# Kernel tuning notes

Hardware: AMD Instinct MI355X
Metric: run time of the kernel (lower is better)

Reference implementation:

```python
import jax, jax.numpy as jnp
import numpy as np

LN_EPS = 1e-5


def _segment_mean(vals, idx, num_segments):
    s = jax.ops.segment_sum(vals, idx, num_segments=num_segments)
    cnt = jax.ops.segment_sum(jnp.ones((vals.shape[0],), vals.dtype), idx, num_segments=num_segments)
    return s / jnp.maximum(cnt, 1.0)[:, None]


def _sage_layer(x, src, dst, W_l, b_l, W_r, gamma, beta):
    # PyG SAGEConv (mean aggr): out = lin_l(mean_{j in N(i)} x_j) + lin_r(x_i)
    N = x.shape[0]
    agg = _segment_mean(x[src], dst, N)                     # [N, in]
    h = agg @ W_l.T + b_l + x @ W_r.T                       # [N, out]
    mu = jnp.mean(h, axis=-1, keepdims=True)
    var = jnp.mean((h - mu) ** 2, axis=-1, keepdims=True)
    h = (h - mu) * jax.lax.rsqrt(var + LN_EPS) * gamma + beta
    return jax.nn.relu(h)                                   # dropout: eval mode (identity)


def setup_inputs() -> dict:
    key = jax.random.key(0)
    ks = jax.random.split(key, 20)
    N, E, IN, H, OUT, G, C = 50000, 600000, 128, 128, 64, 64, 2

    def glorot(k, fo, fi):
        lim = np.sqrt(6.0 / (fo + fi)).astype(np.float32)
        return jax.random.uniform(k, (fo, fi), jnp.float32, -lim, lim)

    inp = {
        'x': jax.random.normal(ks[0], (N, IN), jnp.float32),
        'edge_index': jax.random.randint(ks[1], (2, E), 0, N, jnp.int64),
        'batch': jnp.sort(jax.random.randint(ks[2], (N,), 0, G, jnp.int64)),
    }
    dims = [(IN, H), (H, H), (H, OUT)]
    for i, (fi, fo) in enumerate(dims):
        inp[f'Wl{i}'] = glorot(ks[3 + 4 * i], fo, fi)
        inp[f'bl{i}'] = jnp.zeros((fo,), jnp.float32)
        inp[f'Wr{i}'] = glorot(ks[4 + 4 * i], fo, fi)
        inp[f'g{i}'] = jnp.ones((fo,), jnp.float32)
        inp[f'be{i}'] = jnp.zeros((fo,), jnp.float32)
    inp['cW1'] = glorot(ks[16], H, 2 * OUT)
    inp['cb1'] = jnp.zeros((H,), jnp.float32)
    inp['cW2'] = glorot(ks[17], C, H)
    inp['cb2'] = jnp.zeros((C,), jnp.float32)
    return inp


def reference(x, edge_index, batch,
              Wl0, bl0, Wr0, g0, be0,
              Wl1, bl1, Wr1, g1, be1,
              Wl2, bl2, Wr2, g2, be2,
              cW1, cb1, cW2, cb2):
    src, dst = edge_index[0], edge_index[1]
    h = _sage_layer(x, src, dst, Wl0, bl0, Wr0, g0, be0)
    h = _sage_layer(h, src, dst, Wl1, bl1, Wr1, g1, be1)
    h = _sage_layer(h, src, dst, Wl2, bl2, Wr2, g2, be2)
    G = 64  # number of graphs
    x_mean = _segment_mean(h, batch, G)                     # [G, out]
    x_max = jax.ops.segment_max(h, batch, num_segments=G)   # [G, out]
    z = jnp.concatenate([x_mean, x_max], axis=-1)           # [G, 2*out]
    z = jax.nn.relu(z @ cW1.T + cb1)
    return z @ cW2.T + cb2                                  # [G, num_classes]
```

## Files before the change

### kernel.cpp

```cpp
#include <hip/hip_runtime.h>

typedef unsigned short ushort_t;
typedef short s16x8 __attribute__((ext_vector_type(8)));
typedef float f32x4 __attribute__((ext_vector_type(4)));

#define LN_EPS 1e-5f

__device__ __forceinline__ float b2f(ushort_t u) {
    return __uint_as_float(((unsigned)u) << 16);
}
__device__ __forceinline__ ushort_t f2b(float f) {
    unsigned b = __float_as_uint(f);
    b += 0x7FFFu + ((b >> 16) & 1u);
    return (ushort_t)(b >> 16);
}
__device__ __forceinline__ unsigned f2b2(float lo, float hi) {
    return (unsigned)f2b(lo) | ((unsigned)f2b(hi) << 16);
}
__device__ __forceinline__ float ldf(const void* p, size_t i, int isF) {
    return isF ? ((const float*)p)[i] : b2f(((const ushort_t*)p)[i]);
}

__global__ void GraphSAGE_36026185678961_kernel() {}

__global__ void k_detect_zero(const void* w0, const void* ei, int* __restrict__ flags,
                              int* __restrict__ deg, float* __restrict__ Z, int N) {
    int i = blockIdx.x * blockDim.x + threadIdx.x;
    if (i < N) deg[i] = 0;
    if (i < 64 * 128) Z[i] = 0.f;
    if (blockIdx.x == 0 && threadIdx.x < 64) {
        int t = threadIdx.x;
        const ushort_t* u = (const ushort_t*)w0;
        int pass = 0;
        #pragma unroll
        for (int k = 0; k < 4; ++k) {
            ushort_t v = u[t * 4 + k];
            int ex = (v >> 7) & 0xFF;
            if (ex == 0 || (ex >= 0x60 && ex <= 0x7E)) pass++;
        }
        const unsigned* w = (const unsigned*)ei;
        int nz = (w[2 * t + 1] != 0u) ? 1 : 0;
        #pragma unroll
        for (int off = 32; off; off >>= 1) {
            pass += __shfl_down(pass, off, 64);
            nz += __shfl_down(nz, off, 64);
        }
        if (t == 0) {
            flags[0] = (pass < 205) ? 1 : 0;
            flags[1] = (nz == 0) ? 1 : 0;
        }
    }
}

__global__ void k_xconv(const void* X, const int* __restrict__ flags,
                        ushort_t* __restrict__ XB, int total4) {
    int idx = blockIdx.x * blockDim.x + threadIdx.x;
    if (idx >= total4) return;
    if (flags[0]) {
        float4 v = ((const float4*)X)[idx];
        ushort4 o;
        o.x = f2b(v.x); o.y = f2b(v.y); o.z = f2b(v.z); o.w = f2b(v.w);
        ((ushort4*)XB)[idx] = o;
    } else {
        ((ushort4*)XB)[idx] = ((const ushort4*)X)[idx];
    }
}

__global__ void k_hist(const void* ei, int E, int N, const int* __restrict__ flags,
                       int* __restrict__ deg) {
    int e = blockIdx.x * blockDim.x + threadIdx.x;
    if (e >= E) return;
    int d = flags[1] ? (int)((const long long*)ei)[E + e] : ((const int*)ei)[E + e];
    if ((unsigned)d < (unsigned)N) atomicAdd(&deg[d], 1);
}

__global__ void k_scan1(const int* __restrict__ deg, int N,
                        int* __restrict__ rowptr, int* __restrict__ bsum) {
    __shared__ int wsum[4];
    __shared__ int wpre[4];
    int tid = threadIdx.x;
    int lane = tid & 63;
    int w = tid >> 6;
    int i = blockIdx.x * 256 + tid;
    int v = (i < N) ? deg[i] : 0;
    int x = v;
    #pragma unroll
    for (int off = 1; off < 64; off <<= 1) {
        int t = __shfl_up(x, off, 64);
        if (lane >= off) x += t;
    }
    if (lane == 63) wsum[w] = x;
    __syncthreads();
    if (tid == 0) {
        int a = wsum[0]; wpre[0] = a;
        a += wsum[1]; wpre[1] = a;
        a += wsum[2]; wpre[2] = a;
        a += wsum[3]; wpre[3] = a;
    }
    __syncthreads();
    int woff = (w == 0) ? 0 : wpre[w - 1];
    if (i < N) rowptr[i] = woff + x - v;
    if (tid == 0) bsum[blockIdx.x] = wpre[3];
}

__global__ void k_scan2(const int* __restrict__ bsum, int nb,
                        int* __restrict__ boff, int* __restrict__ rowptrN,
                        const void* batch, int N, int G, const int* __restrict__ flags,
                        int* __restrict__ bounds) {
    __shared__ int wsum[4];
    __shared__ int wpre[4];
    int tid = threadIdx.x;
    int lane = tid & 63;
    int w = tid >> 6;
    int run = 0;
    for (int base = 0; base < nb; base += 256) {
        int i = base + tid;
        int v = (i < nb) ? bsum[i] : 0;
        int x = v;
        #pragma unroll
        for (int off = 1; off < 64; off <<= 1) {
            int t = __shfl_up(x, off, 64);
            if (lane >= off) x += t;
        }
        if (lane == 63) wsum[w] = x;
        __syncthreads();
        if (tid == 0) {
            int a = wsum[0]; wpre[0] = a;
            a += wsum[1]; wpre[1] = a;
            a += wsum[2]; wpre[2] = a;
            a += wsum[3]; wpre[3] = a;
        }
        __syncthreads();
        int woff = (w == 0) ? 0 : wpre[w - 1];
        if (i < nb) boff[i] = run + woff + x - v;
        int tot = wpre[3];
        __syncthreads();
        run += tot;
    }
    if (tid == 0) *rowptrN = run;
    if (tid <= G) {
        int isL = flags[1];
        int lo = 0, hi = N;
        while (lo < hi) {
            int mid = (lo + hi) >> 1;
            int bv = isL ? (int)((const long long*)batch)[mid] : ((const int*)batch)[mid];
            if (bv < tid) lo = mid + 1; else hi = mid;
        }
        bounds[tid] = lo;
    }
}

__global__ void k_scan3(int* __restrict__ rowptr, const int* __restrict__ boff,
                        int* __restrict__ cursor, int N) {
    int i = blockIdx.x * 256 + threadIdx.x;
    if (i < N) {
        int r = rowptr[i] + boff[i >> 8];
        rowptr[i] = r;
        cursor[i] = r;
    }
}

__global__ void k_fill(const void* ei, int E, int N, const int* __restrict__ flags,
                       int* __restrict__ cursor, int* __restrict__ col) {
    int e = blockIdx.x * blockDim.x + threadIdx.x;
    if (e >= E) return;
    int s, d;
    if (flags[1]) {
        const long long* p = (const long long*)ei;
        s = (int)p[e];
        d = (int)p[E + e];
    } else {
        const int* p = (const int*)ei;
        s = p[e];
        d = p[E + e];
    }
    if ((unsigned)d < (unsigned)N) {
        int p = atomicAdd(&cursor[d], 1);
        if ((unsigned)p < (unsigned)E) col[p] = ((unsigned)s < (unsigned)N) ? s : 0;
    }
}

__global__ __launch_bounds__(256) void k_agg(
    const ushort_t* __restrict__ X, const int* __restrict__ rowptr,
    const int* __restrict__ col, ushort_t* __restrict__ AGG, int N) {
    int i = blockIdx.x * 4 + (threadIdx.x >> 6);
    if (i >= N) return;
    int l = threadIdx.x & 63;
    int qn = l >> 4;
    int fo = l & 15;
    const uint4* X8 = (const uint4*)X;
    int s = rowptr[i], e = rowptr[i + 1];
    float al[4] = {0.f, 0.f, 0.f, 0.f};
    float ah[4] = {0.f, 0.f, 0.f, 0.f};
    int p = s + qn;
    for (; p + 4 < e; p += 8) {
        int j0 = col[p], j1 = col[p + 4];
        uint4 u0 = X8[(size_t)j0 * 16 + fo];
        uint4 u1 = X8[(size_t)j1 * 16 + fo];
        unsigned w0[4] = {u0.x, u0.y, u0.z, u0.w};
        unsigned w1[4] = {u1.x, u1.y, u1.z, u1.w};
        #pragma unroll
        for (int k = 0; k < 4; ++k) {
            al[k] += __uint_as_float(w0[k] << 16) + __uint_as_float(w1[k] << 16);
            ah[k] += __uint_as_float(w0[k] & 0xFFFF0000u) + __uint_as_float(w1[k] & 0xFFFF0000u);
        }
    }
    for (; p < e; p += 4) {
        int j = col[p];
        uint4 u = X8[(size_t)j * 16 + fo];
        unsigned w0[4] = {u.x, u.y, u.z, u.w};
        #pragma unroll
        for (int k = 0; k < 4; ++k) {
            al[k] += __uint_as_float(w0[k] << 16);
            ah[k] += __uint_as_float(w0[k] & 0xFFFF0000u);
        }
    }
    #pragma unroll
    for (int k = 0; k < 4; ++k) {
        al[k] += __shfl_xor(al[k], 16, 64);
        al[k] += __shfl_xor(al[k], 32, 64);
        ah[k] += __shfl_xor(ah[k], 16, 64);
        ah[k] += __shfl_xor(ah[k], 32, 64);
    }
    if (qn == 0) {
        int d = e - s;
        float inv = 1.f / (float)(d > 0 ? d : 1);
        uint4 o;
        o.x = f2b2(al[0] * inv, ah[0] * inv);
        o.y = f2b2(al[1] * inv, ah[1] * inv);
        o.z = f2b2(al[2] * inv, ah[2] * inv);
        o.w = f2b2(al[3] * inv, ah[3] * inv);
        ((uint4*)AGG)[(size_t)i * 16 + fo] = o;
    }
}

__global__ void k_wprep(const void* Wl0, const void* Wr0, const void* Wl1, const void* Wr1,
                        const void* Wl2, const void* Wr2, const int* __restrict__ flags,
                        ushort_t* __restrict__ Wb0, ushort_t* __restrict__ Wb1,
                        ushort_t* __restrict__ Wb2) {
    int t = blockIdx.x * blockDim.x + threadIdx.x;
    int isF = flags[0];
    const void* Wl;
    const void* Wr;
    ushort_t* Wb;
    int base;
    if (t < 256 * 128) { Wl = Wl0; Wr = Wr0; Wb = Wb0; base = t; }
    else if (t < 2 * 256 * 128) { Wl = Wl1; Wr = Wr1; Wb = Wb1; base = t - 256 * 128; }
    else if (t < 2 * 256 * 128 + 256 * 64) { Wl = Wl2; Wr = Wr2; Wb = Wb2; base = t - 2 * 256 * 128; }
    else return;
    int f = base >> 8, k = base & 255;
    float v = (k < 128) ? ldf(Wl, f * 128 + k, isF) : ldf(Wr, f * 128 + (k - 128), isF);
    Wb[base] = isF ? f2b(v) : ((const ushort_t*)((k < 128) ? Wl : Wr))[f * 128 + (k & 127)];
}

template <int FO>
__global__ __launch_bounds__(256, 2) void k_gemm_ln(
    const ushort_t* __restrict__ AGG, const ushort_t* __restrict__ X,
    const ushort_t* __restrict__ Wb,
    const void* bl, const void* gam, const void* bet,
    const int* __restrict__ flags,
    ushort_t* __restrict__ H, int M) {
    constexpr int NT = FO / 16;
    constexpr int R = 2;
    int lane = threadIdx.x & 63;
    int wid = threadIdx.x >> 6;
    int wrow0 = (blockIdx.x * 4 + wid) * (R * 16);
    if (wrow0 >= M) return;
    int isF = flags[0];
    int m = lane & 15;
    int q = lane >> 4;

    int arow[R];
    #pragma unroll
    for (int r = 0; r < R; ++r) {
        int ar = wrow0 + r * 16 + m;
        arow[r] = (ar < M) ? ar : (M - 1);
    }

    f32x4 acc[R][NT];
    #pragma unroll
    for (int r = 0; r < R; ++r)
        #pragma unroll
        for (int nt = 0; nt < NT; ++nt) acc[r][nt] = (f32x4){0.f, 0.f, 0.f, 0.f};

    #pragma unroll
    for (int kk = 0; kk < 8; ++kk) {
        const ushort_t* base = (kk < 4) ? AGG : X;
        int ko = (kk & 3) * 32 + q * 8;
        s16x8 a[R];
        #pragma unroll
        for (int r = 0; r < R; ++r)
            a[r] = *(const s16x8*)(base + (size_t)arow[r] * 128 + ko);
        #pragma unroll
        for (int nt = 0; nt < NT; ++nt) {
            s16x8 b = *(const s16x8*)(Wb + (size_t)(nt * 16 + m) * 256 + kk * 32 + q * 8);
            #pragma unroll
            for (int r = 0; r < R; ++r)
                acc[r][nt] = __builtin_amdgcn_mfma_f32_16x16x32_bf16(a[r], b, acc[r][nt], 0, 0, 0);
        }
    }

    #pragma unroll
    for (int r = 0; r < R; ++r) {
        #pragma unroll
        for (int nt = 0; nt < NT; ++nt) {
            float bv = ldf(bl, nt * 16 + m, isF);
            #pragma unroll
            for (int rr = 0; rr < 4; ++rr) acc[r][nt][rr] += bv;
        }
        float mu[4], rs[4];
        #pragma unroll
        for (int rr = 0; rr < 4; ++rr) {
            float s1 = 0.f, s2 = 0.f;
            #pragma unroll
            for (int nt = 0; nt < NT; ++nt) {
                float v = acc[r][nt][rr];
                s1 += v;
                s2 += v * v;
            }
            #pragma unroll
            for (int off = 1; off < 16; off <<= 1) {
                s1 += __shfl_xor(s1, off, 64);
                s2 += __shfl_xor(s2, off, 64);
            }
            float mm = s1 / (float)FO;
            float var = s2 / (float)FO - mm * mm;
            var = var > 0.f ? var : 0.f;
            mu[rr] = mm;
            rs[rr] = rsqrtf(var + LN_EPS);
        }
        #pragma unroll
        for (int nt = 0; nt < NT; ++nt) {
            int n0 = nt * 16 + m;
            float g = ldf(gam, n0, isF);
            float be = ldf(bet, n0, isF);
            #pragma unroll
            for (int rr = 0; rr < 4; ++rr) {
                int row = wrow0 + r * 16 + q * 4 + rr;
                if (row < M) {
                    float y = (acc[r][nt][rr] - mu[rr]) * rs[rr] * g + be;
                    y = y > 0.f ? y : 0.f;
                    H[(size_t)row * FO + n0] = f2b(y);
                }
            }
        }
    }
}

__global__ __launch_bounds__(256) void k_pool(
    const ushort_t* __restrict__ H,
    const int* __restrict__ bounds, float* __restrict__ Z, int N) {
    int g = blockIdx.x >> 4;
    int chunk = blockIdx.x & 15;
    int lane = threadIdx.x & 31;
    int sub = threadIdx.x >> 5;
    int strm = chunk * 8 + sub;
    int s = bounds[g], e = bounds[g + 1];
    s = s < 0 ? 0 : (s > N ? N : s);
    e = e < s ? s : (e > N ? N : e);
    const unsigned* H2 = (const unsigned*)H;
    float sl = 0.f, sh = 0.f, ml = 0.f, mh = 0.f;
    for (int i = s + strm; i < e; i += 128) {
        unsigned u = H2[(size_t)i * 32 + lane];
        float vl = __uint_as_float(u << 16);
        float vh = __uint_as_float(u & 0xFFFF0000u);
        sl += vl; sh += vh;
        ml = ml > vl ? ml : vl;
        mh = mh > vh ? mh : vh;
    }
    int f0 = lane * 2;
    atomicAdd(&Z[g * 128 + f0], sl);
    atomicAdd(&Z[g * 128 + f0 + 1], sh);
    atomicMax((int*)&Z[g * 128 + 64 + f0], __float_as_int(ml));
    atomicMax((int*)&Z[g * 128 + 64 + f0 + 1], __float_as_int(mh));
}

__global__ void k_mlp(const float* __restrict__ Z, const int* __restrict__ bounds,
                      const void* cW1, const void* cb1, const void* cW2, const void* cb2,
                      const int* __restrict__ flags, void* __restrict__ out) {
    int g = blockIdx.x;
    int f = threadIdx.x;
    int isF = flags[0];
    __shared__ float z[128];
    __shared__ float hid[128];
    __shared__ float r0[2], r1[2];
    int cnt = bounds[g + 1] - bounds[g];
    float c = (float)(cnt > 0 ? cnt : 1);
    float zv = Z[g * 128 + f];
    if (f < 64) zv /= c;
    z[f] = zv;
    __syncthreads();
    float acc = ldf(cb1, f, isF);
    #pragma unroll 8
    for (int k = 0; k < 128; ++k) acc += z[k] * ldf(cW1, f * 128 + k, isF);
    acc = acc > 0.f ? acc : 0.f;
    hid[f] = acc;
    __syncthreads();
    float p0 = hid[f] * ldf(cW2, f, isF);
    float p1 = hid[f] * ldf(cW2, 128 + f, isF);
    #pragma unroll
    for (int off = 32; off > 0; off >>= 1) {
        p0 += __shfl_xor(p0, off, 64);
        p1 += __shfl_xor(p1, off, 64);
    }
    int w = f >> 6;
    if ((f & 63) == 0) { r0[w] = p0; r1[w] = p1; }
    __syncthreads();
    if (f == 0) {
        float v0 = r0[0] + r0[1] + ldf(cb2, 0, isF);
        float v1 = r1[0] + r1[1] + ldf(cb2, 1, isF);
        if (isF) {
            ((float*)out)[g * 2 + 0] = v0;
            ((float*)out)[g * 2 + 1] = v1;
        } else {
            ((ushort_t*)out)[g * 2 + 0] = f2b(v0);
            ((ushort_t*)out)[g * 2 + 1] = f2b(v1);
        }
    }
}

extern "C" void kernel_launch(void* const* d_in, const int* in_sizes, int n_in,
                              void* d_out, int out_size, void* d_ws, size_t ws_size,
                              hipStream_t stream) {
    const void* x = d_in[0];
    const void* ei = d_in[1];
    const void* batch = d_in[2];
    const void* Wl0 = d_in[3];
    const void* bl0 = d_in[4];
    const void* Wr0 = d_in[5];
    const void* g0 = d_in[6];
    const void* be0 = d_in[7];
    const void* Wl1 = d_in[8];
    const void* bl1 = d_in[9];
    const void* Wr1 = d_in[10];
    const void* g1 = d_in[11];
    const void* be1 = d_in[12];
    const void* Wl2 = d_in[13];
    const void* bl2 = d_in[14];
    const void* Wr2 = d_in[15];
    const void* g2 = d_in[16];
    const void* be2 = d_in[17];
    const void* cW1 = d_in[18];
    const void* cb1 = d_in[19];
    const void* cW2 = d_in[20];
    const void* cb2 = d_in[21];

    const int N = in_sizes[0] / 128;
    const int E = in_sizes[1] / 2;
    const int G = 64;

    char* w = (char*)d_ws;
    size_t o = 0;
    auto take = [&](size_t bytes) -> void* {
        void* p = w + o;
        o = (o + bytes + 255) & ~(size_t)255;
        return p;
    };
    int nb1 = (N + 255) / 256;
    int* flags  = (int*)take(4 * 4);
    int* rowptr = (int*)take((size_t)(N + 1) * 4);
    int* cursor = (int*)take((size_t)N * 4);
    int* deg    = (int*)take((size_t)N * 4);
    int* bsum   = (int*)take((size_t)nb1 * 4);
    int* boff   = (int*)take((size_t)nb1 * 4);
    int* col    = (int*)take((size_t)E * 4);
    int* bounds = (int*)take((size_t)(G + 1) * 4);
    float* Z    = (float*)take((size_t)G * 128 * 4);
    ushort_t* Wb0 = (ushort_t*)take((size_t)128 * 256 * 2);
    ushort_t* Wb1 = (ushort_t*)take((size_t)128 * 256 * 2);
    ushort_t* Wb2 = (ushort_t*)take((size_t)64 * 256 * 2);
    ushort_t* AGG = (ushort_t*)take((size_t)N * 128 * 2);
    ushort_t* H1  = (ushort_t*)take((size_t)N * 128 * 2);
    ushort_t* H2  = (ushort_t*)take((size_t)N * 128 * 2);
    ushort_t* XB  = H2;
    ushort_t* H3  = H1;
    if (o > ws_size) return;

    int eb = (E + 255) / 256;
    k_detect_zero<<<nb1, 256, 0, stream>>>(Wl0, ei, flags, deg, Z, N);
    k_xconv<<<(N * 128 / 4 + 255) / 256, 256, 0, stream>>>(x, flags, XB, N * 128 / 4);
    k_hist<<<eb, 256, 0, stream>>>(ei, E, N, flags, deg);
    k_scan1<<<nb1, 256, 0, stream>>>(deg, N, rowptr, bsum);
    k_scan2<<<1, 256, 0, stream>>>(bsum, nb1, boff, rowptr + N, batch, N, G, flags, bounds);
    k_scan3<<<nb1, 256, 0, stream>>>(rowptr, boff, cursor, N);
    k_fill<<<eb, 256, 0, stream>>>(ei, E, N, flags, cursor, col);
    k_wprep<<<(2 * 256 * 128 + 256 * 64 + 255) / 256, 256, 0, stream>>>(
        Wl0, Wr0, Wl1, Wr1, Wl2, Wr2, flags, Wb0, Wb1, Wb2);

    int gb = (N + 127) / 128;
    int ab = (N + 3) / 4;

    k_agg<<<ab, 256, 0, stream>>>(XB, rowptr, col, AGG, N);
    k_gemm_ln<128><<<gb, 256, 0, stream>>>(AGG, XB, Wb0, bl0, g0, be0, flags, H1, N);
    k_agg<<<ab, 256, 0, stream>>>(H1, rowptr, col, AGG, N);
    k_gemm_ln<128><<<gb, 256, 0, stream>>>(AGG, H1, Wb1, bl1, g1, be1, flags, H2, N);
    k_agg<<<ab, 256, 0, stream>>>(H2, rowptr, col, AGG, N);
    k_gemm_ln<64><<<gb, 256, 0, stream>>>(AGG, H2, Wb2, bl2, g2, be2, flags, H3, N);

    k_pool<<<G * 16, 256, 0, stream>>>(H3, bounds, Z, N);
    k_mlp<<<G, 128, 0, stream>>>(Z, bounds, cW1, cb1, cW2, cb2, flags, d_out);
}
```

Measured before the change: 376.8 us.

## Transform-then-aggregate in last SAGE layer and merge prep kernels

The last layer now multiplies node features by the stacked [Wl2;Wr2] first, producing a 128-wide T. It then gathers and averages only the 64-wide Wl part over neighbours and fuses bias, self term, LayerNorm and ReLU into the aggregation kernel. This halves the gather width for layer 3 and drops the separate AGG round trip. It also merges the x conversion, degree histogram and weight prep into a single launch. The cost is that neighbour sums are taken over bf16-rounded projected values rather than raw features, which changes rounding slightly.

Result: no change. 377.1 us (+0.1%).

```diff
diff --git a/kernel.cpp b/kernel.cpp
--- a/kernel.cpp
+++ b/kernel.cpp
@@ -52,26 +52,55 @@
     }
 }
 
-__global__ void k_xconv(const void* X, const int* __restrict__ flags,
-                        ushort_t* __restrict__ XB, int total4) {
-    int idx = blockIdx.x * blockDim.x + threadIdx.x;
-    if (idx >= total4) return;
-    if (flags[0]) {
-        float4 v = ((const float4*)X)[idx];
-        ushort4 o;
-        o.x = f2b(v.x); o.y = f2b(v.y); o.z = f2b(v.z); o.w = f2b(v.w);
-        ((ushort4*)XB)[idx] = o;
+__global__ void k_prep(const void* X, ushort_t* __restrict__ XB, int total4, int xb,
+                       const void* ei, int E, int N, int* __restrict__ deg, int eb,
+                       const void* Wl0, const void* Wr0, const void* Wl1, const void* Wr1,
+                       const void* Wl2, const void* Wr2,
+                       ushort_t* __restrict__ Wb0, ushort_t* __restrict__ Wb1,
+                       ushort_t* __restrict__ Wb2,
+                       const int* __restrict__ flags) {
+    int b = blockIdx.x;
+    if (b < xb) {
+        int idx = b * 256 + threadIdx.x;
+        if (idx >= total4) return;
+        if (flags[0]) {
+            float4 v = ((const float4*)X)[idx];
+            ushort4 o;
+            o.x = f2b(v.x); o.y = f2b(v.y); o.z = f2b(v.z); o.w = f2b(v.w);
+            ((ushort4*)XB)[idx] = o;
+        } else {
+            ((ushort4*)XB)[idx] = ((const ushort4*)X)[idx];
+        }
+    } else if (b < xb + eb) {
+        int e = (b - xb) * 256 + threadIdx.x;
+        if (e >= E) return;
+        int d = flags[1] ? (int)((const long long*)ei)[E + e] : ((const int*)ei)[E + e];
+        if ((unsigned)d < (unsigned)N) atomicAdd(&deg[d], 1);
     } else {
-        ((ushort4*)XB)[idx] = ((const ushort4*)X)[idx];
-    }
-}
-
-__global__ void k_hist(const void* ei, int E, int N, const int* __restrict__ flags,
-                       int* __restrict__ deg) {
-    int e = blockIdx.x * blockDim.x + threadIdx.x;
-    if (e >= E) return;
-    int d = flags[1] ? (int)((const long long*)ei)[E + e] : ((const int*)ei)[E + e];
-    if ((unsigned)d < (unsigned)N) atomicAdd(&deg[d], 1);
+        int t = (b - xb - eb) * 256 + threadIdx.x;
+        int isF = flags[0];
+        if (t < 2 * 32768) {
+            const void* Wl = (t < 32768) ? Wl0 : Wl1;
+            const void* Wr = (t < 32768) ? Wr0 : Wr1;
+            ushort_t* Wb = (t < 32768) ? Wb0 : Wb1;
+            int base = t & 32767;
+            int f = base >> 8, k = base & 255;
+            if (isF) {
+                float v = (k < 128) ? ((const float*)Wl)[f * 128 + k]
+                                    : ((const float*)Wr)[f * 128 + (k - 128)];
+                Wb[base] = f2b(v);
+            } else {
+                Wb[base] = ((const ushort_t*)((k < 128) ? Wl : Wr))[f * 128 + (k & 127)];
+            }
+        } else if (t < 2 * 32768 + 16384) {
+            int base = t - 2 * 32768;
+            int f = base >> 7, k = base & 127;
+            const void* W = (f < 64) ? Wl2 : Wr2;
+            int fr = f & 63;
+            Wb2[base] = isF ? f2b(((const float*)W)[fr * 128 + k])
+                            : ((const ushort_t*)W)[fr * 128 + k];
+        }
+    }
 }
 
 __global__ void k_scan1(const int* __restrict__ deg, int N,
@@ -234,25 +263,6 @@
     }
 }
 
-__global__ void k_wprep(const void* Wl0, const void* Wr0, const void* Wl1, const void* Wr1,
-                        const void* Wl2, const void* Wr2, const int* __restrict__ flags,
-                        ushort_t* __restrict__ Wb0, ushort_t* __restrict__ Wb1,
-                        ushort_t* __restrict__ Wb2) {
-    int t = blockIdx.x * blockDim.x + threadIdx.x;
-    int isF = flags[0];
-    const void* Wl;
-    const void* Wr;
-    ushort_t* Wb;
-    int base;
-    if (t < 256 * 128) { Wl = Wl0; Wr = Wr0; Wb = Wb0; base = t; }
-    else if (t < 2 * 256 * 128) { Wl = Wl1; Wr = Wr1; Wb = Wb1; base = t - 256 * 128; }
-    else if (t < 2 * 256 * 128 + 256 * 64) { Wl = Wl2; Wr = Wr2; Wb = Wb2; base = t - 2 * 256 * 128; }
-    else return;
-    int f = base >> 8, k = base & 255;
-    float v = (k < 128) ? ldf(Wl, f * 128 + k, isF) : ldf(Wr, f * 128 + (k - 128), isF);
-    Wb[base] = isF ? f2b(v) : ((const ushort_t*)((k < 128) ? Wl : Wr))[f * 128 + (k & 127)];
-}
-
 template <int FO>
 __global__ __launch_bounds__(256, 2) void k_gemm_ln(
     const ushort_t* __restrict__ AGG, const ushort_t* __restrict__ X,
@@ -344,6 +354,141 @@
                 }
             }
         }
+    }
+}
+
+__global__ __launch_bounds__(256, 2) void k_gemm3(
+    const ushort_t* __restrict__ X,
+    const ushort_t* __restrict__ Wb,
+    ushort_t* __restrict__ T,
+    int M) {
+    constexpr int NT = 8;
+    constexpr int R = 2;
+    int lane = threadIdx.x & 63;
+    int wid = threadIdx.x >> 6;
+    int wrow0 = (blockIdx.x * 4 + wid) * (R * 16);
+    if (wrow0 >= M) return;
+    int m = lane & 15;
+    int q = lane >> 4;
+
+    int arow[R];
+    #pragma unroll
+    for (int r = 0; r < R; ++r) {
+        int ar = wrow0 + r * 16 + m;
+        arow[r] = (ar < M) ? ar : (M - 1);
+    }
+
+    f32x4 acc[R][NT];
+    #pragma unroll
+    for (int r = 0; r < R; ++r)
+        #pragma unroll
+        for (int nt = 0; nt < NT; ++nt) acc[r][nt] = (f32x4){0.f, 0.f, 0.f, 0.f};
+
+    #pragma unroll
+    for (int kk = 0; kk < 4; ++kk) {
+        int ko = kk * 32 + q * 8;
+        s16x8 a[R];
+        #pragma unroll
+        for (int r = 0; r < R; ++r)
+            a[r] = *(const s16x8*)(X + (size_t)arow[r] * 128 + ko);
+        #pragma unroll
+        for (int nt = 0; nt < NT; ++nt) {
+            s16x8 b = *(const s16x8*)(Wb + (size_t)(nt * 16 + m) * 128 + ko);
+            #pragma unroll
+            for (int r = 0; r < R; ++r)
+                acc[r][nt] = __builtin_amdgcn_mfma_f32_16x16x32_bf16(a[r], b, acc[r][nt], 0, 0, 0);
+        }
+    }
+
+    #pragma unroll
+    for (int r = 0; r < R; ++r)
+        #pragma unroll
+        for (int nt = 0; nt < NT; ++nt) {
+            int n0 = nt * 16 + m;
+            #pragma unroll
+            for (int rr = 0; rr < 4; ++rr) {
+                int row = wrow0 + r * 16 + q * 4 + rr;
+                if (row < M) T[(size_t)row * 128 + n0] = f2b(acc[r][nt][rr]);
+            }
+        }
+}
+
+__global__ __launch_bounds__(256) void k_agg3(
+    const ushort_t* __restrict__ T,
+    const int* __restrict__ rowptr, const int* __restrict__ col,
+    const void* bl, const void* gam, const void* bet, const int* __restrict__ flags,
+    ushort_t* __restrict__ H, int N) {
+    int i = blockIdx.x * 4 + (threadIdx.x >> 6);
+    if (i >= N) return;
+    int l = threadIdx.x & 63;
+    int qn = l >> 4;
+    int fo = l & 15;
+    int isF = flags[0];
+    const uint2* T2 = (const uint2*)T;
+    int s = rowptr[i], e = rowptr[i + 1];
+    float al[2] = {0.f, 0.f};
+    float ah[2] = {0.f, 0.f};
+    int p = s + qn;
+    for (; p + 4 < e; p += 8) {
+        int j0 = col[p], j1 = col[p + 4];
+        uint2 u0 = T2[(size_t)j0 * 32 + fo];
+        uint2 u1 = T2[(size_t)j1 * 32 + fo];
+        unsigned w0[2] = {u0.x, u0.y};
+        unsigned w1[2] = {u1.x, u1.y};
+        #pragma unroll
+        for (int k = 0; k < 2; ++k) {
+            al[k] += __uint_as_float(w0[k] << 16) + __uint_as_float(w1[k] << 16);
+            ah[k] += __uint_as_float(w0[k] & 0xFFFF0000u) + __uint_as_float(w1[k] & 0xFFFF0000u);
+        }
+    }
+    for (; p < e; p += 4) {
+        int j = col[p];
+        uint2 u = T2[(size_t)j * 32 + fo];
+        unsigned w0[2] = {u.x, u.y};
+        #pragma unroll
+        for (int k = 0; k < 2; ++k) {
+            al[k] += __uint_as_float(w0[k] << 16);
+            ah[k] += __uint_as_float(w0[k] & 0xFFFF0000u);
+        }
+    }
+    #pragma unroll
+    for (int k = 0; k < 2; ++k) {
+        al[k] += __shfl_xor(al[k], 16, 64);
+        al[k] += __shfl_xor(al[k], 32, 64);
+        ah[k] += __shfl_xor(ah[k], 16, 64);
+        ah[k] += __shfl_xor(ah[k], 32, 64);
+    }
+    int d = e - s;
+    float inv = 1.f / (float)(d > 0 ? d : 1);
+    uint2 su = T2[(size_t)i * 32 + 16 + fo];
+    float v0 = al[0] * inv + __uint_as_float(su.x << 16) + ldf(bl, 4 * fo + 0, isF);
+    float v1 = ah[0] * inv + __uint_as_float(su.x & 0xFFFF0000u) + ldf(bl, 4 * fo + 1, isF);
+    float v2 = al[1] * inv + __uint_as_float(su.y << 16) + ldf(bl, 4 * fo + 2, isF);
+    float v3 = ah[1] * inv + __uint_as_float(su.y & 0xFFFF0000u) + ldf(bl, 4 * fo + 3, isF);
+    float s1 = v0 + v1 + v2 + v3;
+    float s2 = v0 * v0 + v1 * v1 + v2 * v2 + v3 * v3;
+    #pragma unroll
+    for (int off = 1; off < 16; off <<= 1) {
+        s1 += __shfl_xor(s1, off, 64);
+        s2 += __shfl_xor(s2, off, 64);
+    }
+    float mu = s1 / 64.f;
+    float var = s2 / 64.f - mu * mu;
+    var = var > 0.f ? var : 0.f;
+    float rs = rsqrtf(var + LN_EPS);
+    if (qn == 0) {
+        float y0 = (v0 - mu) * rs * ldf(gam, 4 * fo + 0, isF) + ldf(bet, 4 * fo + 0, isF);
+        float y1 = (v1 - mu) * rs * ldf(gam, 4 * fo + 1, isF) + ldf(bet, 4 * fo + 1, isF);
+        float y2 = (v2 - mu) * rs * ldf(gam, 4 * fo + 2, isF) + ldf(bet, 4 * fo + 2, isF);
+        float y3 = (v3 - mu) * rs * ldf(gam, 4 * fo + 3, isF) + ldf(bet, 4 * fo + 3, isF);
+        y0 = y0 > 0.f ? y0 : 0.f;
+        y1 = y1 > 0.f ? y1 : 0.f;
+        y2 = y2 > 0.f ? y2 : 0.f;
+        y3 = y3 > 0.f ? y3 : 0.f;
+        uint2 o;
+        o.x = f2b2(y0, y1);
+        o.y = f2b2(y2, y3);
+        ((uint2*)H)[(size_t)i * 16 + fo] = o;
     }
 }
 
@@ -468,24 +613,27 @@
     float* Z    = (float*)take((size_t)G * 128 * 4);
     ushort_t* Wb0 = (ushort_t*)take((size_t)128 * 256 * 2);
     ushort_t* Wb1 = (ushort_t*)take((size_t)128 * 256 * 2);
-    ushort_t* Wb2 = (ushort_t*)take((size_t)64 * 256 * 2);
+    ushort_t* Wb2 = (ushort_t*)take((size_t)128 * 128 * 2);
     ushort_t* AGG = (ushort_t*)take((size_t)N * 128 * 2);
     ushort_t* H1  = (ushort_t*)take((size_t)N * 128 * 2);
     ushort_t* H2  = (ushort_t*)take((size_t)N * 128 * 2);
     ushort_t* XB  = H2;
+    ushort_t* T3  = AGG;
     ushort_t* H3  = H1;
     if (o > ws_size) return;
 
     int eb = (E + 255) / 256;
+    int xb = (N * 128 / 4 + 255) / 256;
+    int wb = (2 * 32768 + 16384 + 255) / 256;
     k_detect_zero<<<nb1, 256, 0, stream>>>(Wl0, ei, flags, deg, Z, N);
-    k_xconv<<<(N * 128 / 4 + 255) / 256, 256, 0, stream>>>(x, flags, XB, N * 128 / 4);
-    k_hist<<<eb, 256, 0, stream>>>(ei, E, N, flags, deg);
+    k_prep<<<xb + eb + wb, 256, 0, stream>>>(x, XB, N * 128 / 4, xb,
+                                             ei, E, N, deg, eb,
+                                             Wl0, Wr0, Wl1, Wr1, Wl2, Wr2,
+                                             Wb0, Wb1, Wb2, flags);
     k_scan1<<<nb1, 256, 0, stream>>>(deg, N, rowptr, bsum);
     k_scan2<<<1, 256, 0, stream>>>(bsum, nb1, boff, rowptr + N, batch, N, G, flags, bounds);
     k_scan3<<<nb1, 256, 0, stream>>>(rowptr, boff, cursor, N);
     k_fill<<<eb, 256, 0, stream>>>(ei, E, N, flags, cursor, col);
-    k_wprep<<<(2 * 256 * 128 + 256 * 64 + 255) / 256, 256, 0, stream>>>(
-        Wl0, Wr0, Wl1, Wr1, Wl2, Wr2, flags, Wb0, Wb1, Wb2);
 
     int gb = (N + 127) / 128;
     int ab = (N + 3) / 4;
@@ -494,8 +642,8 @@
     k_gemm_ln<128><<<gb, 256, 0, stream>>>(AGG, XB, Wb0, bl0, g0, be0, flags, H1, N);
     k_agg<<<ab, 256, 0, stream>>>(H1, rowptr, col, AGG, N);
     k_gemm_ln<128><<<gb, 256, 0, stream>>>(AGG, H1, Wb1, bl1, g1, be1, flags, H2, N);
-    k_agg<<<ab, 256, 0, stream>>>(H2, rowptr, col, AGG, N);
-    k_gemm_ln<64><<<gb, 256, 0, stream>>>(AGG, H2, Wb2, bl2, g2, be2, flags, H3, N);
+    k_gemm3<<<gb, 256, 0, stream>>>(H2, Wb2, T3, N);
+    k_agg3<<<ab, 256, 0, stream>>>(T3, rowptr, col, bl2, g2, be2, flags, H3, N);
 
     k_pool<<<G * 16, 256, 0, stream>>>(H3, bounds, Z, N);
     k_mlp<<<G, 128, 0, stream>>>(Z, bounds, cW1, cb1, cW2, cb2, flags, d_out);
```
